# Kernel tuning notes

Measured on AMD Instinct MI355X. Metric: run time of the kernel, lower is better.

The kernel has to match this reference:

```python
import jax, jax.numpy as jnp
import numpy as np
import math

EPS = 1e-6
P_MIN = 1e-3
P_MAX = 10.0
NUM_ITERS = 3
REG = 1.0
K = 64       # num_clusters
D = 128      # cluster_dim
TOKEN = 256  # token_dim
B, N, C = 8, 8192, 512


def _l2norm(t):
    return t / jnp.clip(jnp.linalg.norm(t, axis=-1, keepdims=True), 1e-12)


def _mlp(h, W1, b1, W2, b2):
    # torch Linear: y = h @ W.T + b ; dropout is identity at eval
    return jax.nn.relu(h @ W1.T + b1) @ W2.T + b2


def _log_otp_solver(log_a, log_b, M, num_iters, reg):
    M = M / reg
    u = jnp.zeros_like(log_a)
    v = jnp.zeros_like(log_b)
    for _ in range(num_iters):  # fixed small iteration count
        u = log_a - jax.scipy.special.logsumexp(M + v[:, None, :], axis=2)
        v = log_b - jax.scipy.special.logsumexp(M + u[:, :, None], axis=1)
    return M + u[:, :, None] + v[:, None, :]


def _get_matching_probs(S, dustbin_score, num_iters, reg):
    b, m, n = S.shape
    dust_row = jnp.broadcast_to(dustbin_score, (b, 1, n)).astype(S.dtype)
    S_aug = jnp.concatenate([S, dust_row], axis=1)  # [b, m+1, n]
    norm = -math.log(n + m)
    log_a = jnp.full((m + 1,), norm, dtype=S.dtype).at[-1].add(math.log(n - m))
    log_a = jnp.broadcast_to(log_a, (b, m + 1))
    log_b = jnp.full((b, n), norm, dtype=S.dtype)
    log_P = _log_otp_solver(log_a, log_b, S_aug, num_iters, reg)
    return log_P - norm


def setup_inputs() -> dict:
    key = jax.random.key(0)
    ks = jax.random.split(key, 8)
    x = jax.random.normal(ks[0], (B, N, C), dtype=jnp.float32)

    def lin(k, fin, fout):
        k1, k2 = jax.random.split(k)
        W = 0.02 * jax.random.normal(k1, (fout, fin), dtype=jnp.float32)
        b = 0.02 * jax.random.normal(k2, (fout,), dtype=jnp.float32)
        return W, b

    tW1, tb1 = lin(ks[1], C, 512)
    tW2, tb2 = lin(ks[2], 512, TOKEN)
    cW1, cb1 = lin(ks[3], C, 512)
    cW2, cb2 = lin(ks[4], 512, D)
    sW1, sb1 = lin(ks[5], C, 512)
    sW2, sb2 = lin(ks[6], 512, K)
    # GeM p param init so that softplus(w)+p_min == 3.0
    gem_w = jnp.array([math.log(math.exp(3.0 - P_MIN) - 1.0)], dtype=jnp.float32)
    dust_bin = jnp.array(1.0, dtype=jnp.float32)
    return dict(x=x, gem_w=gem_w, dust_bin=dust_bin,
                tW1=tW1, tb1=tb1, tW2=tW2, tb2=tb2,
                cW1=cW1, cb1=cb1, cW2=cW2, cb2=cb2,
                sW1=sW1, sb1=sb1, sW2=sW2, sb2=sb2)


def reference(x, gem_w, dust_bin,
              tW1, tb1, tW2, tb2,
              cW1, cb1, cW2, cb2,
              sW1, sb1, sW2, sb2):
    # --- GeM pooling: [B, N, C] -> [B, C] ---
    p = jnp.minimum(jax.nn.softplus(gem_w) + P_MIN, P_MAX)  # [1]
    g = jnp.mean(jnp.clip(x.astype(jnp.float32), EPS, None) ** p, axis=1) ** (1.0 / p)
    g = jnp.where(jnp.isfinite(g), g, jnp.zeros_like(g))

    global_token = _mlp(g, tW1, tb1, tW2, tb2)          # [B, TOKEN]
    local = _mlp(x, cW1, cb1, cW2, cb2)                 # [B, N, D]
    scores = _mlp(x, sW1, sb1, sW2, sb2)                # [B, N, K]

    S = scores.transpose(0, 2, 1)                       # [B, K, N]
    log_P = _get_matching_probs(S, dust_bin, NUM_ITERS, REG)  # [B, K+1, N]
    p_mat = jnp.exp(log_P)[:, :-1, :]                   # drop dustbin -> [B, K, N]

    # aggregated[b, d, k] = sum_n local[b, n, d] * p[b, k, n]  (no O(B*D*K*N) blowup)
    agg = jnp.einsum('bnd,bkn->bdk', local, p_mat).reshape(x.shape[0], -1)  # [B, D*K]

    result = jnp.concatenate([_l2norm(global_token), _l2norm(agg)], axis=-1)
    return _l2norm(result)
```

## Files before the change

kernel.cpp:

```cpp
#include <hip/hip_runtime.h>
#include <hip/hip_bf16.h>
#include <math.h>

#define BB   8
#define NN   8192
#define CC   512
#define DD   128
#define KK   64
#define TOK  256
#define MM   (BB*NN)

typedef unsigned short u16;
typedef __attribute__((ext_vector_type(8))) short short8;
typedef __attribute__((ext_vector_type(4))) float floatx4;

struct PtrSz { const void* p[15]; int sz[15]; };

__device__ __forceinline__ float bf2f(u16 v) {
    union { unsigned u; float f; } x; x.u = ((unsigned)v) << 16; return x.f;
}
__device__ __forceinline__ u16 f2bf(float f) {
    union { float f; unsigned u; } x; x.f = f;
    unsigned r = x.u + 0x7fffu + ((x.u >> 16) & 1u);
    return (u16)(r >> 16);
}
__device__ __forceinline__ float nat_exp2(float a) {
    float r; asm("v_exp_f32 %0, %1" : "=v"(r) : "v"(a)); return r;
}
__device__ __forceinline__ float nat_log2(float a) {
    float r; asm("v_log_f32 %0, %1" : "=v"(r) : "v"(a)); return r;
}
__device__ __forceinline__ void gload16(const void* g, void* l) {
    __builtin_amdgcn_global_load_lds(
        (const __attribute__((address_space(1))) void*)g,
        (__attribute__((address_space(3))) void*)l, 16, 0, 0);
}

__global__ __launch_bounds__(256)
void fill_sentinel(float* __restrict__ out, int n, float val) {
    int i = blockIdx.x*256 + threadIdx.x;
    if (i < n) out[i] = val;
}

__global__ __launch_bounds__(256)
void detect_all(PtrSz ps, int* __restrict__ flags) {
    int i = blockIdx.x;
    const u16* q = (const u16*)ps.p[i];
    int m = ps.sz[i] < 4096 ? ps.sz[i] : 4096;
    __shared__ int cnt;
    if (threadIdx.x == 0) cnt = 0;
    __syncthreads();
    int c = 0;
    for (int j = threadIdx.x; j < m; j += 256) {
        int e = (q[j] >> 7) & 0xFF;
        if (e < 90 || e > 165) c++;
    }
    atomicAdd(&cnt, c);
    __syncthreads();
    if (threadIdx.x == 0) flags[i] = (cnt * 8 > m) ? 1 : 0;
}

#define W_TW1 0
#define W_TB1 262144
#define W_TW2 262656
#define W_TB2 393728
#define W_CW1 393984
#define W_CB1 656128
#define W_CW2 656640
#define W_CB2 722176
#define W_SW1 722304
#define W_SB1 984448
#define W_SW2 984960
#define W_SB2 1017728
#define W_TOTAL 1017792

__global__ __launch_bounds__(256)
void conv_weights(PtrSz ps, const int* __restrict__ flags,
                  u16* __restrict__ wbuf, float* __restrict__ wscal) {
    long gid = (long)blockIdx.x*256 + threadIdx.x;
    if (gid == 0) {
        float vb = bf2f(((const u16*)ps.p[1])[0]);
        float vf = ((const float*)ps.p[1])[0];
        wscal[0] = (fabsf(vb - 2.94694f) < 0.2f) ? vb : vf;
    } else if (gid == 1) {
        float vb = bf2f(((const u16*)ps.p[2])[0]);
        float vf = ((const float*)ps.p[2])[0];
        wscal[1] = (fabsf(vb - 1.0f) < 0.2f) ? vb : vf;
    }
    if (gid >= W_TOTAL) return;
    int idx; long off;
    if      (gid < W_TB1) { idx = 3;  off = W_TW1; }
    else if (gid < W_TW2) { idx = 4;  off = W_TB1; }
    else if (gid < W_TB2) { idx = 5;  off = W_TW2; }
    else if (gid < W_CW1) { idx = 6;  off = W_TB2; }
    else if (gid < W_CB1) { idx = 7;  off = W_CW1; }
    else if (gid < W_CW2) { idx = 8;  off = W_CB1; }
    else if (gid < W_CB2) { idx = 9;  off = W_CW2; }
    else if (gid < W_SW1) { idx = 10; off = W_CB2; }
    else if (gid < W_SB1) { idx = 11; off = W_SW1; }
    else if (gid < W_SW2) { idx = 12; off = W_SB1; }
    else if (gid < W_SB2) { idx = 13; off = W_SW2; }
    else                  { idx = 14; off = W_SB2; }
    long k = gid - off;
    bool f32in = flags[idx] != 0;
    wbuf[gid] = f32in ? f2bf(((const float*)ps.p[idx])[k]) : ((const u16*)ps.p[idx])[k];
}

__global__ __launch_bounds__(256)
void gem_partial(const void* __restrict__ x, const float* __restrict__ wscal,
                 const int* __restrict__ flags, float* __restrict__ gacc) {
    __shared__ float red[4][512];
    int b = blockIdx.x, ny = blockIdx.y;
    int tid  = threadIdx.x;
    int wave = tid >> 6, lane = tid & 63;
    bool f32in = (flags[0] != 0);
    float gw = wscal[0];
    float p  = fminf(log1pf(expf(gw)) + 1e-3f, 10.0f);
    int c0 = lane*8;
    float s[8];
#pragma unroll
    for (int j = 0; j < 8; ++j) s[j] = 0.f;
    size_t base = ((size_t)b*NN + (size_t)ny*64 + wave)*CC + c0;
    if (f32in) {
        const float* xf = (const float*)x;
#pragma unroll 4
        for (int n = 0; n < 64; n += 4) {
            const float* pf = xf + base + (size_t)n*CC;
            float4 x0 = *(const float4*)pf;
            float4 x1 = *(const float4*)(pf + 4);
            float xv[8] = {x0.x,x0.y,x0.z,x0.w,x1.x,x1.y,x1.z,x1.w};
#pragma unroll
            for (int j = 0; j < 8; ++j)
                s[j] += nat_exp2(p * nat_log2(fmaxf(xv[j], 1e-6f)));
        }
    } else {
        const u16* xu = (const u16*)x;
#pragma unroll 4
        for (int n = 0; n < 64; n += 4) {
            short8 v8 = *(const short8*)(xu + base + (size_t)n*CC);
#pragma unroll
            for (int j = 0; j < 8; ++j)
                s[j] += nat_exp2(p * nat_log2(fmaxf(bf2f((u16)v8[j]), 1e-6f)));
        }
    }
#pragma unroll
    for (int j = 0; j < 8; ++j) red[wave][c0 + j] = s[j];
    __syncthreads();
#pragma unroll
    for (int t = 0; t < 2; ++t) {
        int c = tid + t*256;
        float v = red[0][c] + red[1][c] + red[2][c] + red[3][c];
        atomicAdd(&gacc[b*CC + c], v);
    }
}

__global__ __launch_bounds__(512)
void token_mlp(const float* __restrict__ gacc, const u16* __restrict__ wbuf,
               const float* __restrict__ wscal, float* __restrict__ t) {
    __shared__ float gs[CC];
    __shared__ float hs[512];
    int b = blockIdx.x, j = threadIdx.x;
    {
        float gw = wscal[0];
        float p  = fminf(log1pf(expf(gw)) + 1e-3f, 10.0f);
        float m  = gacc[b*CC + j] / (float)NN;
        float r  = powf(m, 1.0f/p);
        if (!isfinite(r)) r = 0.f;
        gs[j] = r;
    }
    __syncthreads();
    {
        float a = bf2f(wbuf[W_TB1 + j]);
        const u16* w = wbuf + W_TW1 + (size_t)j*CC;
        for (int c = 0; c < CC; c += 8) {
            short8 wv = *(const short8*)(w + c);
#pragma unroll
            for (int q = 0; q < 8; ++q) a += gs[c+q]*bf2f((u16)wv[q]);
        }
        hs[j] = fmaxf(a, 0.f);
    }
    __syncthreads();
    if (j < TOK) {
        float a2 = bf2f(wbuf[W_TB2 + j]);
        const u16* w2 = wbuf + W_TW2 + (size_t)j*512;
        for (int c = 0; c < 512; c += 8) {
            short8 wv = *(const short8*)(w2 + c);
#pragma unroll
            for (int q = 0; q < 8; ++q) a2 += hs[c+q]*bf2f((u16)wv[q]);
        }
        t[b*TOK + j] = a2;
    }
}

template<int BN, int MODE, bool RELU, bool ARAW>
__global__ __launch_bounds__(256)
void gemm_bt(const void* __restrict__ A, const u16* __restrict__ W,
             const u16* __restrict__ bias, void* __restrict__ Cout,
             const int* __restrict__ flags, int N, int Ksz, int lda,
             size_t a_base, int bidx_ovr,
             const u16* __restrict__ W_alt, const u16* __restrict__ bias_alt,
             int nsplit) {
    constexpr int WSUB_N = BN/32;
    constexpr int APARTS = 4;
    constexpr int BPARTS = BN/32;
    extern __shared__ char smem[];
    u16* a_lds = (u16*)smem;
    u16* b_lds = (u16*)smem + 128*64;
    const int tid  = threadIdx.x;
    const int wave = tid >> 6, lane = tid & 63;
    const int wm = wave >> 1, wn = wave & 1;

    int bx = blockIdx.x, by = blockIdx.y;
    {
        int nbx = gridDim.x, nby = gridDim.y;
        int nwg = nbx*nby;
        if ((nwg & 7) == 0) {
            int lid = bx + by*nbx;
            int q = nwg >> 3;
            int t = (lid & 7)*q + (lid >> 3);
            by = t % nby;
            bx = t / nby;
        }
    }
    const u16* Wp = W; const u16* bp = bias;
    int byw = by;
    if (W_alt != nullptr && by >= nsplit) { Wp = W_alt; bp = bias_alt; byw = by - nsplit; }
    const int bm0 = bx * 128;
    const int bn0 = by * BN;
    const int bw0 = byw * BN;
    const int fr = lane & 15;
    const int fk = (lane >> 4) * 8;
    const bool f32in = ARAW && (flags[0] != 0);

    floatx4 acc[4][WSUB_N];
#pragma unroll
    for (int i = 0; i < 4; ++i)
#pragma unroll
        for (int j = 0; j < WSUB_N; ++j) acc[i][j] = (floatx4){0.f,0.f,0.f,0.f};

    for (int k0 = 0; k0 < Ksz; k0 += 64) {
        if (f32in) {
#pragma unroll
            for (int part = 0; part < APARTS; ++part) {
                int l = part*256 + tid;
                int row = l >> 3, kc = (l & 7)*8;
                size_t gidx = a_base + (size_t)(bm0 + row)*lda + k0 + kc;
                const float* pf = (const float*)A + gidx;
                float4 x0 = *(const float4*)pf;
                float4 x1 = *(const float4*)(pf + 4);
                short8 vA;
                vA[0]=(short)f2bf(x0.x); vA[1]=(short)f2bf(x0.y);
                vA[2]=(short)f2bf(x0.z); vA[3]=(short)f2bf(x0.w);
                vA[4]=(short)f2bf(x1.x); vA[5]=(short)f2bf(x1.y);
                vA[6]=(short)f2bf(x1.z); vA[7]=(short)f2bf(x1.w);
                int dst = l ^ ((l >> 3) & 7);
                *(short8*)(a_lds + dst*8) = vA;
            }
        } else {
#pragma unroll
            for (int part = 0; part < APARTS; ++part) {
                int cb = part*256 + wave*64;
                int tc = cb + lane;
                int s  = tc ^ ((tc >> 3) & 7);
                int row = s >> 3, kc = (s & 7)*8;
                gload16((const u16*)A + a_base + (size_t)(bm0 + row)*lda + k0 + kc,
                        a_lds + (size_t)cb*8);
            }
        }
#pragma unroll
        for (int part = 0; part < BPARTS; ++part) {
            int cb = part*256 + wave*64;
            int tc = cb + lane;
            int s  = tc ^ ((tc >> 3) & 7);
            int row = s >> 3, kc = (s & 7)*8;
            gload16(Wp + (size_t)(bw0 + row)*Ksz + k0 + kc,
                    b_lds + (size_t)cb*8);
        }
        __syncthreads();
#pragma unroll
        for (int kk = 0; kk < 2; ++kk) {
            short8 af[4], bfr[WSUB_N];
#pragma unroll
            for (int i = 0; i < 4; ++i) {
                int row = wm*64 + i*16 + fr;
                af[i] = *(const short8*)(a_lds + row*64 + ((kk*32 + fk) ^ ((row & 7) << 3)));
            }
#pragma unroll
            for (int j = 0; j < WSUB_N; ++j) {
                int row = wn*WSUB_N*16 + j*16 + fr;
                bfr[j] = *(const short8*)(b_lds + row*64 + ((kk*32 + fk) ^ ((row & 7) << 3)));
            }
#pragma unroll
            for (int i = 0; i < 4; ++i)
#pragma unroll
                for (int j = 0; j < WSUB_N; ++j)
                    acc[i][j] = __builtin_amdgcn_mfma_f32_16x16x32_bf16(af[i], bfr[j], acc[i][j], 0, 0, 0);
        }
        __syncthreads();
    }

    if constexpr (MODE == 0) {
        u16* C = (u16*)Cout;
#pragma unroll
        for (int i = 0; i < 4; ++i) {
            int row0 = wm*64 + i*16 + ((lane>>4)<<2);
#pragma unroll
            for (int j = 0; j < WSUB_N; ++j) {
                int col = wn*WSUB_N*16 + j*16 + fr;
                float bb = bf2f(bp[bw0+col]);
#pragma unroll
                for (int r = 0; r < 4; ++r) {
                    float v = acc[i][j][r] + bb;
                    if (RELU) v = fmaxf(v, 0.f);
                    C[(size_t)(bm0+row0+r)*N + (bn0+col)] = f2bf(v);
                }
            }
        }
    } else {
        const int bidx = (bidx_ovr >= 0) ? bidx_ovr : (bm0 >> 13);
        const int nin  = bm0 & 8191;
        if constexpr (MODE == 1) {
            u16* tr = (u16*)smem;
#pragma unroll
            for (int i = 0; i < 4; ++i) {
                int row0 = wm*64 + i*16 + ((lane>>4)<<2);
#pragma unroll
                for (int j = 0; j < WSUB_N; ++j) {
                    int col = wn*WSUB_N*16 + j*16 + fr;
                    float bb = bf2f(bp[bw0+col]);
#pragma unroll
                    for (int r = 0; r < 4; ++r) {
                        float v = acc[i][j][r] + bb;
                        if (RELU) v = fmaxf(v, 0.f);
                        tr[col*128 + row0 + r] = f2bf(v);
                    }
                }
            }
            __syncthreads();
            u16* O = (u16*)Cout;
#pragma unroll
            for (int c = 0; c < (BN*128)/256; ++c) {
                int flat = c*256 + tid;
                int dcol = flat >> 7, rr = flat & 127;
                O[(size_t)(bidx*BN + bn0 + dcol)*NN + nin + rr] = tr[dcol*128 + rr];
            }
        } else {
            float* tr = (float*)smem;
#pragma unroll
            for (int i = 0; i < 4; ++i) {
                int row0 = wm*64 + i*16 + ((lane>>4)<<2);
#pragma unroll
                for (int j = 0; j < WSUB_N; ++j) {
                    int col = wn*WSUB_N*16 + j*16 + fr;
                    float bb = bf2f(bp[bw0+col]);
#pragma unroll
                    for (int r = 0; r < 4; ++r) {
                        float v = acc[i][j][r] + bb;
                        if (RELU) v = fmaxf(v, 0.f);
                        tr[col*128 + row0 + r] = v;
                    }
                }
            }
            __syncthreads();
            float* O = (float*)Cout;
#pragma unroll
            for (int c = 0; c < (BN*128)/256; ++c) {
                int flat = c*256 + tid;
                int dcol = flat >> 7, rr = flat & 127;
                O[(size_t)(bidx*BN + bn0 + dcol)*NN + nin + rr] = tr[dcol*128 + rr];
            }
        }
    }
}

__global__ __launch_bounds__(256)
void sink_u(const float* __restrict__ ST, const float* __restrict__ v,
            const float* __restrict__ wscal, float* __restrict__ u) {
    int m = blockIdx.x, b = blockIdx.y, t = threadIdx.x;
    const float norm = -logf(8256.0f);
    float la = (m == 64) ? norm + logf(8128.0f) : norm;
    float dustf = wscal[1];
    const float* vb = v + (size_t)b*NN;
    float r[32];
    float mx = -1e30f;
    if (m < 64) {
        const float* row = ST + ((size_t)b*64 + m)*NN;
#pragma unroll
        for (int i = 0; i < 32; ++i) { int n = t + i*256; r[i] = row[n] + vb[n]; mx = fmaxf(mx, r[i]); }
    } else {
#pragma unroll
        for (int i = 0; i < 32; ++i) { int n = t + i*256; r[i] = dustf + vb[n]; mx = fmaxf(mx, r[i]); }
    }
#pragma unroll
    for (int off = 32; off; off >>= 1) mx = fmaxf(mx, __shfl_xor(mx, off));
    __shared__ float red[4];
    if ((t & 63) == 0) red[t>>6] = mx;
    __syncthreads();
    mx = fmaxf(fmaxf(red[0], red[1]), fmaxf(red[2], red[3]));
    __syncthreads();
    float s = 0.f;
#pragma unroll
    for (int i = 0; i < 32; ++i) s += expf(r[i] - mx);
#pragma unroll
    for (int off = 32; off; off >>= 1) s += __shfl_xor(s, off);
    if ((t & 63) == 0) red[t>>6] = s;
    __syncthreads();
    s = red[0] + red[1] + red[2] + red[3];
    if (t == 0) u[b*65 + m] = la - (mx + logf(s));
}

template<int WP>
__global__ __launch_bounds__(256)
void sink_v_t(const float* __restrict__ ST, const float* __restrict__ u,
              const float* __restrict__ wscal, float* __restrict__ v,
              u16* __restrict__ P) {
    int b = blockIdx.y;
    int n = blockIdx.x*256 + threadIdx.x;
    __shared__ float us[65];
    if (threadIdx.x < 65) us[threadIdx.x] = u[b*65 + threadIdx.x];
    __syncthreads();
    const float norm = -logf(8256.0f);
    float mx = wscal[1] + us[64];
    float s  = 1.0f;
    const float* col = ST + (size_t)b*64*NN + n;
    if (WP) {
        float r[64];
#pragma unroll
        for (int m = 0; m < 64; ++m) {
            r[m] = col[(size_t)m*NN] + us[m];
            float nm = fmaxf(mx, r[m]);
            s = s*expf(mx - nm) + expf(r[m] - nm);
            mx = nm;
        }
        float vn = norm - (mx + logf(s));
        v[(size_t)b*NN + n] = vn;
#pragma unroll
        for (int k = 0; k < 64; ++k)
            P[((size_t)b*64 + k)*NN + n] = f2bf(expf(r[k] + vn - norm));
    } else {
        for (int m = 0; m < 64; ++m) {
            float tv = col[(size_t)m*NN] + us[m];
            float nm = fmaxf(mx, tv);
            s = s*expf(mx - nm) + expf(tv - nm);
            mx = nm;
        }
        v[(size_t)b*NN + n] = norm - (mx + logf(s));
    }
}

__global__ __launch_bounds__(256)
void agg_mfma(const u16* __restrict__ localT, const u16* __restrict__ P,
              float* __restrict__ agg) {
    __shared__ u16 a_lds[128*32];
    __shared__ u16 b_lds[64*32];
    int b = blockIdx.y, ns = blockIdx.x;
    int n0 = ns*256;
    const int tid  = threadIdx.x;
    const int wave = tid >> 6, lane = tid & 63;
    const int wm = wave >> 1, wn = wave & 1;
    const int fr = lane & 15, fk = (lane >> 4)*8;

    floatx4 acc[4][2];
#pragma unroll
    for (int i = 0; i < 4; ++i)
#pragma unroll
        for (int j = 0; j < 2; ++j) acc[i][j] = (floatx4){0.f,0.f,0.f,0.f};

    for (int s = 0; s < 8; ++s) {
        int nk = n0 + s*32;
#pragma unroll
        for (int part = 0; part < 2; ++part) {
            int chunk = part*256 + tid;
            int row = chunk >> 2, kc = (chunk & 3)*8;
            short8 vA = *(const short8*)(localT + ((size_t)b*128 + row)*NN + nk + kc);
            *(short8*)(a_lds + row*32 + kc) = vA;
        }
        {
            int row = tid >> 2, kc = (tid & 3)*8;
            short8 vB = *(const short8*)(P + ((size_t)b*64 + row)*NN + nk + kc);
            *(short8*)(b_lds + row*32 + kc) = vB;
        }
        __syncthreads();
        short8 af[4], bfr[2];
#pragma unroll
        for (int i = 0; i < 4; ++i)
            af[i] = *(const short8*)(a_lds + (wm*64 + i*16 + fr)*32 + fk);
#pragma unroll
        for (int j = 0; j < 2; ++j)
            bfr[j] = *(const short8*)(b_lds + (wn*32 + j*16 + fr)*32 + fk);
#pragma unroll
        for (int i = 0; i < 4; ++i)
#pragma unroll
            for (int j = 0; j < 2; ++j)
                acc[i][j] = __builtin_amdgcn_mfma_f32_16x16x32_bf16(af[i], bfr[j], acc[i][j], 0, 0, 0);
        __syncthreads();
    }
#pragma unroll
    for (int i = 0; i < 4; ++i) {
        int d0 = wm*64 + i*16 + ((lane>>4)<<2);
#pragma unroll
        for (int j = 0; j < 2; ++j) {
            int k = wn*32 + j*16 + fr;
#pragma unroll
            for (int r = 0; r < 4; ++r)
                atomicAdd(&agg[(size_t)b*8192 + (d0+r)*64 + k], acc[i][j][r]);
        }
    }
}

__global__ __launch_bounds__(256)
void finalize_out(const float* __restrict__ tg, const float* __restrict__ agg,
                  float* __restrict__ out) {
    int b = blockIdx.x, tid = threadIdx.x;
    float tv = tg[b*TOK + tid];
    float s1 = tv*tv;
    const float* ab = agg + (size_t)b*8192;
    float av[32];
    float s2 = 0.f;
#pragma unroll
    for (int i = 0; i < 32; ++i) { av[i] = ab[tid + i*256]; s2 += av[i]*av[i]; }
#pragma unroll
    for (int off = 32; off; off >>= 1) { s1 += __shfl_xor(s1, off); s2 += __shfl_xor(s2, off); }
    __shared__ float r1[4], r2[4];
    int wave = tid >> 6, lane = tid & 63;
    if (lane == 0) { r1[wave] = s1; r2[wave] = s2; }
    __syncthreads();
    float S1 = r1[0]+r1[1]+r1[2]+r1[3];
    float S2 = r2[0]+r2[1]+r2[2]+r2[3];
    const float rs2 = 1.41421356237f;
    float sc1 = 1.0f/(fmaxf(sqrtf(S1), 1e-12f)*rs2);
    float sc2 = 1.0f/(fmaxf(sqrtf(S2), 1e-12f)*rs2);
    out[(size_t)b*8448 + tid] = tv*sc1;
#pragma unroll
    for (int i = 0; i < 32; ++i)
        out[(size_t)b*8448 + 256 + tid + i*256] = av[i]*sc2;
}

extern "C" void kernel_launch(void* const* d_in, const int* in_sizes, int n_in,
                              void* d_out, int out_size, void* d_ws, size_t ws_size,
                              hipStream_t stream) {
    float* out = (float*)d_out;

    static const int EXP[15] = {33554432,1,1,262144,512,131072,256,
                                262144,512,65536,128,262144,512,32768,64};
    bool ok = (n_in == 15) && (out_size == 67584);
    if (ok) for (int i = 0; i < 15; ++i) ok = ok && (in_sizes[i] == EXP[i]);
    if (!ok) {
        fill_sentinel<<<264, 256, 0, stream>>>(out, out_size, 0.25f);
        return;
    }
    const size_t NEED_BATCH = 52934656ull;
    if (ws_size < NEED_BATCH) {
        fill_sentinel<<<264, 256, 0, stream>>>(out, out_size, 0.5f);
        return;
    }

    const void* x = d_in[0];
    PtrSz ps;
    for (int i = 0; i < 15; ++i) { ps.p[i] = d_in[i]; ps.sz[i] = in_sizes[i]; }

    char* base = (char*)d_ws;
    float* gacc = (float*)(base + 0);
    float* u    = (float*)(base + 16384);
    float* v    = (float*)(base + 18464);
    float* agg  = (float*)(base + 280608);
    const size_t ZERO_BYTES = 542752;
    float* tglb = (float*)(base + 559136);
    int*   flags= (int*)  (base + 567328);
    float* wscal= (float*)(base + 567392);
    u16*   wbuf = (u16*)  (base + 567424);
    float* ST   = (float*)(base + 2603008);
    u16* localT = (u16*)  (base + 19380224);
    u16* P      = (u16*)  (base + 36157440);
    u16* h1     = (u16*)  (base + 44546048);
    const size_t FULL_NEED  = 44546048ull + 67108864ull;
    const size_t FUSED_NEED = 44546048ull + 134217728ull;
    const bool fused = (ws_size >= FUSED_NEED);
    const bool mono  = (ws_size >= FULL_NEED);

    hipMemsetAsync(d_ws, 0, ZERO_BYTES, stream);

    detect_all<<<15, 256, 0, stream>>>(ps, flags);
    conv_weights<<<3977, 256, 0, stream>>>(ps, flags, wbuf, wscal);

    gem_partial<<<dim3(BB, 128), 256, 0, stream>>>(x, wscal, flags, gacc);
    token_mlp<<<BB, 512, 0, stream>>>(gacc, wbuf, wscal, tglb);

    const int NOSPLIT = 1 << 30;
    if (fused) {
        gemm_bt<128, 0, true,  true ><<<dim3(512, 8), 256, 32768, stream>>>(
            x, wbuf + W_CW1, wbuf + W_CB1, h1, flags, 1024, 512, 512, 0, -1,
            wbuf + W_SW1, wbuf + W_SB1, 4);
        gemm_bt<128, 1, false, false><<<dim3(512, 1), 256, 32768, stream>>>(
            h1, wbuf + W_CW2, wbuf + W_CB2, localT, flags, 128, 512, 1024, 0, -1,
            nullptr, nullptr, NOSPLIT);
        gemm_bt< 64, 2, false, false><<<dim3(512, 1), 256, 32768, stream>>>(
            h1, wbuf + W_SW2, wbuf + W_SB2, ST, flags, 64, 512, 1024, 512, -1,
            nullptr, nullptr, NOSPLIT);
    } else if (mono) {
        gemm_bt<128, 0, true,  true ><<<dim3(512, 4), 256, 32768, stream>>>(
            x, wbuf + W_CW1, wbuf + W_CB1, h1, flags, 512, 512, 512, 0, -1,
            nullptr, nullptr, NOSPLIT);
        gemm_bt<128, 1, false, false><<<dim3(512, 1), 256, 32768, stream>>>(
            h1, wbuf + W_CW2, wbuf + W_CB2, localT, flags, 128, 512, 512, 0, -1,
            nullptr, nullptr, NOSPLIT);
        gemm_bt<128, 0, true,  true ><<<dim3(512, 4), 256, 32768, stream>>>(
            x, wbuf + W_SW1, wbuf + W_SB1, h1, flags, 512, 512, 512, 0, -1,
            nullptr, nullptr, NOSPLIT);
        gemm_bt< 64, 2, false, false><<<dim3(512, 1), 256, 32768, stream>>>(
            h1, wbuf + W_SW2, wbuf + W_SB2, ST, flags, 64, 512, 512, 0, -1,
            nullptr, nullptr, NOSPLIT);
    } else {
        for (int b = 0; b < BB; ++b) {
            size_t ab = (size_t)b*NN*CC;
            gemm_bt<128, 0, true,  true ><<<dim3(64, 4), 256, 32768, stream>>>(
                x, wbuf + W_CW1, wbuf + W_CB1, h1, flags, 512, 512, 512, ab, -1,
                nullptr, nullptr, NOSPLIT);
            gemm_bt<128, 1, false, false><<<dim3(64, 1), 256, 32768, stream>>>(
                h1, wbuf + W_CW2, wbuf + W_CB2, localT, flags, 128, 512, 512, 0, b,
                nullptr, nullptr, NOSPLIT);
            gemm_bt<128, 0, true,  true ><<<dim3(64, 4), 256, 32768, stream>>>(
                x, wbuf + W_SW1, wbuf + W_SB1, h1, flags, 512, 512, 512, ab, -1,
                nullptr, nullptr, NOSPLIT);
            gemm_bt< 64, 2, false, false><<<dim3(64, 1), 256, 32768, stream>>>(
                h1, wbuf + W_SW2, wbuf + W_SB2, ST, flags, 64, 512, 512, 0, b,
                nullptr, nullptr, NOSPLIT);
        }
    }

    for (int it = 0; it < 3; ++it) {
        sink_u<<<dim3(65, BB), 256, 0, stream>>>(ST, v, wscal, u);
        if (it == 2)
            sink_v_t<1><<<dim3(32, BB), 256, 0, stream>>>(ST, u, wscal, v, P);
        else
            sink_v_t<0><<<dim3(32, BB), 256, 0, stream>>>(ST, u, wscal, v, P);
    }

    agg_mfma<<<dim3(32, BB), 256, 0, stream>>>(localT, P, agg);
    finalize_out<<<BB, 256, 0, stream>>>(tglb, agg, out);
}
```

Baseline: 509.5 us.

## Double-buffer LDS tiles in bf16 GEMM to overlap global loads with MFMA

Adds a second LDS buffer pair to the bf16-input path of gemm_bt, so the next 64-wide K tile is fetched with direct-to-LDS loads while MFMAs consume the current tile. Each step ends with a single fence (vmcnt wait plus barrier) instead of two syncthreads. Dynamic shared memory grows to 64KB (48KB for BN=64), which may lower occupancy per CU. The fp32-input path keeps the single-buffer loop.

New measurement: 593.1 us. +16.4%, slower.

```diff
diff --git a/kernel.cpp b/kernel.cpp
--- a/kernel.cpp
+++ b/kernel.cpp
@@ -204,8 +204,10 @@
     constexpr int APARTS = 4;
     constexpr int BPARTS = BN/32;
     extern __shared__ char smem[];
-    u16* a_lds = (u16*)smem;
-    u16* b_lds = (u16*)smem + 128*64;
+    u16* a0 = (u16*)smem;
+    u16* b0 = a0 + 128*64;
+    u16* a1 = b0 + (size_t)BN*64;
+    u16* b1 = a1 + 128*64;
     const int tid  = threadIdx.x;
     const int wave = tid >> 6, lane = tid & 63;
     const int wm = wave >> 1, wn = wave & 1;
@@ -238,8 +240,67 @@
 #pragma unroll
         for (int j = 0; j < WSUB_N; ++j) acc[i][j] = (floatx4){0.f,0.f,0.f,0.f};
 
-    for (int k0 = 0; k0 < Ksz; k0 += 64) {
-        if (f32in) {
+    auto STAGE = [&](u16* ab, u16* bb, int k0) {
+#pragma unroll
+        for (int part = 0; part < APARTS; ++part) {
+            int cb = part*256 + wave*64;
+            int tc = cb + lane;
+            int s  = tc ^ ((tc >> 3) & 7);
+            int row = s >> 3, kc = (s & 7)*8;
+            gload16((const u16*)A + a_base + (size_t)(bm0 + row)*lda + k0 + kc,
+                    ab + (size_t)cb*8);
+        }
+#pragma unroll
+        for (int part = 0; part < BPARTS; ++part) {
+            int cb = part*256 + wave*64;
+            int tc = cb + lane;
+            int s  = tc ^ ((tc >> 3) & 7);
+            int row = s >> 3, kc = (s & 7)*8;
+            gload16(Wp + (size_t)(bw0 + row)*Ksz + k0 + kc,
+                    bb + (size_t)cb*8);
+        }
+    };
+    auto COMPUTE = [&](const u16* ab, const u16* bb) {
+#pragma unroll
+        for (int kk = 0; kk < 2; ++kk) {
+            short8 af[4], bfr[WSUB_N];
+#pragma unroll
+            for (int i = 0; i < 4; ++i) {
+                int row = wm*64 + i*16 + fr;
+                af[i] = *(const short8*)(ab + row*64 + ((kk*32 + fk) ^ ((row & 7) << 3)));
+            }
+#pragma unroll
+            for (int j = 0; j < WSUB_N; ++j) {
+                int row = wn*WSUB_N*16 + j*16 + fr;
+                bfr[j] = *(const short8*)(bb + row*64 + ((kk*32 + fk) ^ ((row & 7) << 3)));
+            }
+#pragma unroll
+            for (int i = 0; i < 4; ++i)
+#pragma unroll
+                for (int j = 0; j < WSUB_N; ++j)
+                    acc[i][j] = __builtin_amdgcn_mfma_f32_16x16x32_bf16(af[i], bfr[j], acc[i][j], 0, 0, 0);
+        }
+    };
+    auto FENCE = [&]() {
+        __builtin_amdgcn_sched_barrier(0);
+        asm volatile("s_waitcnt vmcnt(0)" ::: "memory");
+        __builtin_amdgcn_s_barrier();
+        __builtin_amdgcn_sched_barrier(0);
+    };
+
+    if (!f32in) {
+        STAGE(a0, b0, 0);
+        FENCE();
+        for (int k0 = 0; k0 < Ksz; k0 += 128) {
+            if (k0 + 64 < Ksz) STAGE(a1, b1, k0 + 64);
+            COMPUTE(a0, b0);
+            FENCE();
+            if (k0 + 128 < Ksz) STAGE(a0, b0, k0 + 128);
+            if (k0 + 64 < Ksz) COMPUTE(a1, b1);
+            FENCE();
+        }
+    } else {
+        for (int k0 = 0; k0 < Ksz; k0 += 64) {
 #pragma unroll
             for (int part = 0; part < APARTS; ++part) {
                 int l = part*256 + tid;
@@ -254,49 +315,21 @@
                 vA[4]=(short)f2bf(x1.x); vA[5]=(short)f2bf(x1.y);
                 vA[6]=(short)f2bf(x1.z); vA[7]=(short)f2bf(x1.w);
                 int dst = l ^ ((l >> 3) & 7);
-                *(short8*)(a_lds + dst*8) = vA;
-            }
-        } else {
-#pragma unroll
-            for (int part = 0; part < APARTS; ++part) {
+                *(short8*)(a0 + dst*8) = vA;
+            }
+#pragma unroll
+            for (int part = 0; part < BPARTS; ++part) {
                 int cb = part*256 + wave*64;
                 int tc = cb + lane;
                 int s  = tc ^ ((tc >> 3) & 7);
                 int row = s >> 3, kc = (s & 7)*8;
-                gload16((const u16*)A + a_base + (size_t)(bm0 + row)*lda + k0 + kc,
-                        a_lds + (size_t)cb*8);
-            }
-        }
-#pragma unroll
-        for (int part = 0; part < BPARTS; ++part) {
-            int cb = part*256 + wave*64;
-            int tc = cb + lane;
-            int s  = tc ^ ((tc >> 3) & 7);
-            int row = s >> 3, kc = (s & 7)*8;
-            gload16(Wp + (size_t)(bw0 + row)*Ksz + k0 + kc,
-                    b_lds + (size_t)cb*8);
-        }
-        __syncthreads();
-#pragma unroll
-        for (int kk = 0; kk < 2; ++kk) {
-            short8 af[4], bfr[WSUB_N];
-#pragma unroll
-            for (int i = 0; i < 4; ++i) {
-                int row = wm*64 + i*16 + fr;
-                af[i] = *(const short8*)(a_lds + row*64 + ((kk*32 + fk) ^ ((row & 7) << 3)));
-            }
-#pragma unroll
-            for (int j = 0; j < WSUB_N; ++j) {
-                int row = wn*WSUB_N*16 + j*16 + fr;
-                bfr[j] = *(const short8*)(b_lds + row*64 + ((kk*32 + fk) ^ ((row & 7) << 3)));
-            }
-#pragma unroll
-            for (int i = 0; i < 4; ++i)
-#pragma unroll
-                for (int j = 0; j < WSUB_N; ++j)
-                    acc[i][j] = __builtin_amdgcn_mfma_f32_16x16x32_bf16(af[i], bfr[j], acc[i][j], 0, 0, 0);
-        }
-        __syncthreads();
+                gload16(Wp + (size_t)(bw0 + row)*Ksz + k0 + kc,
+                        b0 + (size_t)cb*8);
+            }
+            __syncthreads();
+            COMPUTE(a0, b0);
+            __syncthreads();
+        }
     }
 
     if constexpr (MODE == 0) {
@@ -588,41 +621,41 @@
 
     const int NOSPLIT = 1 << 30;
     if (fused) {
-        gemm_bt<128, 0, true,  true ><<<dim3(512, 8), 256, 32768, stream>>>(
+        gemm_bt<128, 0, true,  true ><<<dim3(512, 8), 256, 65536, stream>>>(
             x, wbuf + W_CW1, wbuf + W_CB1, h1, flags, 1024, 512, 512, 0, -1,
             wbuf + W_SW1, wbuf + W_SB1, 4);
-        gemm_bt<128, 1, false, false><<<dim3(512, 1), 256, 32768, stream>>>(
+        gemm_bt<128, 1, false, false><<<dim3(512, 1), 256, 65536, stream>>>(
             h1, wbuf + W_CW2, wbuf + W_CB2, localT, flags, 128, 512, 1024, 0, -1,
             nullptr, nullptr, NOSPLIT);
-        gemm_bt< 64, 2, false, false><<<dim3(512, 1), 256, 32768, stream>>>(
+        gemm_bt< 64, 2, false, false><<<dim3(512, 1), 256, 49152, stream>>>(
             h1, wbuf + W_SW2, wbuf + W_SB2, ST, flags, 64, 512, 1024, 512, -1,
             nullptr, nullptr, NOSPLIT);
     } else if (mono) {
-        gemm_bt<128, 0, true,  true ><<<dim3(512, 4), 256, 32768, stream>>>(
+        gemm_bt<128, 0, true,  true ><<<dim3(512, 4), 256, 65536, stream>>>(
             x, wbuf + W_CW1, wbuf + W_CB1, h1, flags, 512, 512, 512, 0, -1,
             nullptr, nullptr, NOSPLIT);
-        gemm_bt<128, 1, false, false><<<dim3(512, 1), 256, 32768, stream>>>(
+        gemm_bt<128, 1, false, false><<<dim3(512, 1), 256, 65536, stream>>>(
             h1, wbuf + W_CW2, wbuf + W_CB2, localT, flags, 128, 512, 512, 0, -1,
             nullptr, nullptr, NOSPLIT);
-        gemm_bt<128, 0, true,  true ><<<dim3(512, 4), 256, 32768, stream>>>(
+        gemm_bt<128, 0, true,  true ><<<dim3(512, 4), 256, 65536, stream>>>(
             x, wbuf + W_SW1, wbuf + W_SB1, h1, flags, 512, 512, 512, 0, -1,
             nullptr, nullptr, NOSPLIT);
-        gemm_bt< 64, 2, false, false><<<dim3(512, 1), 256, 32768, stream>>>(
+        gemm_bt< 64, 2, false, false><<<dim3(512, 1), 256, 49152, stream>>>(
             h1, wbuf + W_SW2, wbuf + W_SB2, ST, flags, 64, 512, 512, 0, -1,
             nullptr, nullptr, NOSPLIT);
     } else {
         for (int b = 0; b < BB; ++b) {
             size_t ab = (size_t)b*NN*CC;
-            gemm_bt<128, 0, true,  true ><<<dim3(64, 4), 256, 32768, stream>>>(
+            gemm_bt<128, 0, true,  true ><<<dim3(64, 4), 256, 65536, stream>>>(
                 x, wbuf + W_CW1, wbuf + W_CB1, h1, flags, 512, 512, 512, ab, -1,
                 nullptr, nullptr, NOSPLIT);
-            gemm_bt<128, 1, false, false><<<dim3(64, 1), 256, 32768, stream>>>(
+            gemm_bt<128, 1, false, false><<<dim3(64, 1), 256, 65536, stream>>>(
                 h1, wbuf + W_CW2, wbuf + W_CB2, localT, flags, 128, 512, 512, 0, b,
                 nullptr, nullptr, NOSPLIT);
-            gemm_bt<128, 0, true,  true ><<<dim3(64, 4), 256, 32768, stream>>>(
+            gemm_bt<128, 0, true,  true ><<<dim3(64, 4), 256, 65536, stream>>>(
                 x, wbuf + W_SW1, wbuf + W_SB1, h1, flags, 512, 512, 512, ab, -1,
                 nullptr, nullptr, NOSPLIT);
-            gemm_bt< 64, 2, false, false><<<dim3(64, 1), 256, 32768, stream>>>(
+            gemm_bt< 64, 2, false, false><<<dim3(64, 1), 256, 49152, stream>>>(
                 h1, wbuf + W_SW2, wbuf + W_SB2, ST, flags, 64, 512, 512, 0, b,
                 nullptr, nullptr, NOSPLIT);
         }
```
